# Kernel optimization log

Hardware: AMD Instinct MI355X
Metric: run time of the kernel (lower is better)

Reference implementation:

```python
import jax, jax.numpy as jnp
import numpy as np

NHEAD = 16
NEG = -1e9


def sinusoidal_pe(L, D):
    pos = jnp.arange(L, dtype=jnp.float32)[:, None]
    i = jnp.arange(0, D, 2, dtype=jnp.float32)[None, :]
    angle = pos / jnp.power(10000.0, i / D)
    pe = jnp.zeros((L, D), dtype=jnp.float32)
    pe = pe.at[:, 0::2].set(jnp.sin(angle))
    pe = pe.at[:, 1::2].set(jnp.cos(angle))
    return pe


def layer_norm(x, g, b, eps=1e-5):
    m = jnp.mean(x, axis=-1, keepdims=True)
    v = jnp.var(x, axis=-1, keepdims=True)
    return (x - m) * jax.lax.rsqrt(v + eps) * g + b


def build_mixed_mask_local(utt_mask, spk_mask, window, bidirectional=True):
    # utt_mask, spk_mask: [L] ints. Returns three [L, L] bool masks (True = attend).
    L = utt_mask.shape[0]
    idx = jnp.arange(L)
    d = idx[None, :] - idx[:, None]  # j - i
    if bidirectional:
        win = jnp.abs(d) <= window
    else:
        win = (d <= 0) & (d >= -window)
    valid = (utt_mask[None, :] > 0) & (utt_mask[:, None] > 0)
    base = win & valid
    same = spk_mask[None, :] == spk_mask[:, None]
    eye = jnp.eye(L, dtype=bool)
    uttm = base
    samm = base & same
    othm = base & (~same | eye)  # keep self so no query row is fully masked
    return uttm, samm, othm


def encoder_branch(x, bias, Wqkv, bqkv, Wo, bo, g1, b1, Wf1, bf1, Wf2, bf2, g2, b2):
    # x: [L, D]; bias: [L, L] additive mask; stacked per-layer params (leading dim = num_layer)
    num_layer = Wqkv.shape[0]
    L, D = x.shape
    dh = D // NHEAD
    scale = 1.0 / np.sqrt(dh).astype(np.float32)
    for l in range(num_layer):
        qkv = x @ Wqkv[l] + bqkv[l]                       # [L, 3D]
        q, k, v = jnp.split(qkv, 3, axis=-1)
        q = q.reshape(L, NHEAD, dh).transpose(1, 0, 2)    # [H, L, dh]
        k = k.reshape(L, NHEAD, dh).transpose(1, 0, 2)
        v = v.reshape(L, NHEAD, dh).transpose(1, 0, 2)
        s = jnp.einsum('hqd,hkd->hqk', q, k) * scale + bias[None]  # [H, L, L]
        a = jax.nn.softmax(s, axis=-1)
        o = jnp.einsum('hqk,hkd->hqd', a, v).transpose(1, 0, 2).reshape(L, D)
        x = layer_norm(x + o @ Wo[l] + bo[l], g1[l], b1[l])
        f = jax.nn.relu(x @ Wf1[l] + bf1[l]) @ Wf2[l] + bf2[l]
        x = layer_norm(x + f, g2[l], b2[l])
    return x


def fusion_attention(h, W, b, v):
    # h: [K, L, D] -> attention weights over K branch dim
    s = jnp.tanh(h @ W + b) @ v          # [K, L]
    w = jax.nn.softmax(s, axis=0)
    return jnp.einsum('kl,kld->ld', w, h)


def _xavier(key, shape):
    s = np.sqrt(2.0 / (shape[-2] + shape[-1])).astype(np.float32)
    return jax.random.normal(key, shape, dtype=jnp.float32) * s


def setup_inputs() -> dict:
    L, D, DF, NL, C = 1024, 1024, 4096, 3, 7
    key = jax.random.key(0)
    ks = jax.random.split(key, 12)
    return {
        'src': jax.random.normal(ks[0], (L, D), dtype=jnp.float32),
        'utt_mask': jnp.ones((L,), dtype=jnp.int32),
        'spk_mask': jax.random.randint(ks[1], (L,), 0, 2),
        'window': 100,
        'Wqkv': _xavier(ks[2], (3, NL, D, 3 * D)),
        'bqkv': jnp.zeros((3, NL, 3 * D), jnp.float32),
        'Wo': _xavier(ks[3], (3, NL, D, D)),
        'bo': jnp.zeros((3, NL, D), jnp.float32),
        'ln1_g': jnp.ones((3, NL, D), jnp.float32),
        'ln1_b': jnp.zeros((3, NL, D), jnp.float32),
        'Wf1': _xavier(ks[4], (3, NL, D, DF)),
        'bf1': jnp.zeros((3, NL, DF), jnp.float32),
        'Wf2': _xavier(ks[5], (3, NL, DF, D)),
        'bf2': jnp.zeros((3, NL, D), jnp.float32),
        'ln2_g': jnp.ones((3, NL, D), jnp.float32),
        'ln2_b': jnp.zeros((3, NL, D), jnp.float32),
        'f1_W': _xavier(ks[6], (D, D)),
        'f1_b': jnp.zeros((D,), jnp.float32),
        'f1_v': jax.random.normal(ks[7], (D,), dtype=jnp.float32) * 0.02,
        'f2_W': _xavier(ks[8], (D, D)),
        'f2_b': jnp.zeros((D,), jnp.float32),
        'f2_v': jax.random.normal(ks[9], (D,), dtype=jnp.float32) * 0.02,
        'cls_W': _xavier(ks[10], (D, C)),
        'cls_b': jnp.zeros((C,), jnp.float32),
    }


def reference(src, utt_mask, spk_mask, window, Wqkv, bqkv, Wo, bo, ln1_g, ln1_b,
              Wf1, bf1, Wf2, bf2, ln2_g, ln2_b, f1_W, f1_b, f1_v,
              f2_W, f2_b, f2_v, cls_W, cls_b):
    L, D = src.shape
    uttm, samm, othm = build_mixed_mask_local(utt_mask, spk_mask, window, bidirectional=True)
    bias = jnp.where(jnp.stack([uttm, samm, othm]), 0.0, NEG)  # [3, L, L]
    x = src + sinusoidal_pe(L, D)
    outs = jax.vmap(encoder_branch, in_axes=(None, 0, 0, 0, 0, 0, 0, 0, 0, 0, 0, 0, 0, 0))(
        x, bias, Wqkv, bqkv, Wo, bo, ln1_g, ln1_b, Wf1, bf1, Wf2, bf2, ln2_g, ln2_b)
    ct, sm, om = outs[0], outs[1], outs[2]
    sp = fusion_attention(jnp.stack([sm, om]), f1_W, f1_b, f1_v)
    out = fusion_attention(jnp.stack([ct, sp]), f2_W, f2_b, f2_v)
    return jax.nn.log_softmax(out @ cls_W + cls_b, axis=-1)
```

## Files before the change

### kernel.cpp

```cpp
#include <hip/hip_runtime.h>
#include <cmath>

namespace {

constexpr int L   = 1024;
constexpr int D   = 1024;
constexpr int DFF = 4096;
constexpr int NL  = 3;
constexpr int NH  = 16;
constexpr int DH  = 64;
constexpr long LD = (long)L * D;

typedef __attribute__((ext_vector_type(8))) short bf16x8;
typedef __attribute__((ext_vector_type(4))) float f32x4;

__device__ inline void split1(float f, unsigned short& h, unsigned short& l)
{
    unsigned u = __float_as_uint(f);
    h = (unsigned short)(u >> 16);
    float hf = __uint_as_float(u & 0xffff0000u);
    l = (unsigned short)(__float_as_uint(f - hf) >> 16);
}

__device__ inline void xcd_decode(int& bx, int& by, int& bz)
{
    const int gx = gridDim.x, gy = gridDim.y;
    const int nwg = gx * gy * gridDim.z;
    int flat = blockIdx.x + gx * (blockIdx.y + gy * blockIdx.z);
    int w = (flat & 7) * (nwg >> 3) + (flat >> 3);
    bz = w / (gx * gy);
    int rem = w - bz * gx * gy;
    by = rem / gx;
    bx = rem - by * gx;
}

__global__ __launch_bounds__(256)
void repack_w(const float* __restrict__ W, int ldw, long sW,
              unsigned short* __restrict__ out, long sOut, int Np)
{
    const int t    = threadIdx.x;
    const int lane = t & 63;
    const int c    = blockIdx.x * 4 + (t >> 6);
    const int z    = blockIdx.y;
    const int nch  = Np >> 4;
    const int k0   = (c / nch) * 32 + ((lane >> 4) << 3);
    const int n    = (c % nch) * 16 + (lane & 15);
    const float* Wz = W + (long)z * sW + n;
    unsigned short* oz = out + (long)z * sOut + (long)c * 1024 + (lane << 3);
    unsigned short h[8], l[8];
#pragma unroll
    for (int e = 0; e < 8; ++e)
        split1(Wz[(long)(k0 + e) * ldw], h[e], l[e]);
    *(ushort4*)(oz)       = *(ushort4*)&h[0];
    *(ushort4*)(oz + 4)   = *(ushort4*)&h[4];
    *(ushort4*)(oz + 512) = *(ushort4*)&l[0];
    *(ushort4*)(oz + 516) = *(ushort4*)&l[4];
}

template<int BM, int BN, int ACT>
__global__ __launch_bounds__(256)
void gemm_mfma_pb(const float* __restrict__ A, int lda, long sA,
                  const unsigned short* __restrict__ Bp, int Np, long sBp,
                  float* __restrict__ C, int ldc, long sC,
                  const float* __restrict__ bias, long sBias,
                  int K, float alpha, int ksl, long sSlice)
{
    constexpr int BK = 32;
    constexpr int PK = 40;
    constexpr int FM = BM / 32;
    constexpr int FN = BN / 32;
    constexpr int NA = BM / 32;

    __shared__ __align__(16) unsigned short Ah0[BM][PK], Al0[BM][PK];
    __shared__ __align__(16) unsigned short Ah1[BM][PK], Al1[BM][PK];

    int bx, by, bz;
    xcd_decode(bx, by, bz);
    const int zb = bz / ksl, ks = bz - zb * ksl;
    const int kLen = K / ksl, k0 = ks * kLen;
    const int nit = kLen / BK;

    const int tid  = threadIdx.x;
    const int lane = tid & 63;
    const int wave = tid >> 6;
    const int wm   = (wave >> 1) * (BM / 2);
    const int wn   = (wave & 1)  * (BN / 2);
    const int lr   = lane & 15;
    const int ko   = (lane >> 4) * 8;

    const float* Abase = A + (long)zb * sA;
    const unsigned short* Bb = Bp + (long)zb * sBp;
    float* Cbase = C + (long)zb * sC + (long)ks * sSlice;
    const int n0  = bx * BN;
    const int m0  = by * BM;
    const int nch = Np >> 4;
    const int cb  = (n0 + wn) >> 4;

    f32x4 acc[FM][FN];
#pragma unroll
    for (int i = 0; i < FM; ++i)
#pragma unroll
        for (int j = 0; j < FN; ++j) acc[i][j] = f32x4{0.f, 0.f, 0.f, 0.f};

    const int akq = tid & 7;
    const int amr = tid >> 3;

    auto loadA = [&](int kt, float4* pa) {
#pragma unroll
        for (int r = 0; r < NA; ++r)
            pa[r] = *(const float4*)(Abase + (long)(m0 + r * 32 + amr) * lda + kt + akq * 4);
    };
    auto storeA = [&](unsigned short (*AhD)[PK], unsigned short (*AlD)[PK],
                      const float4* pa) {
#pragma unroll
        for (int r = 0; r < NA; ++r) {
            ushort4 h, l;
            split1(pa[r].x, h.x, l.x); split1(pa[r].y, h.y, l.y);
            split1(pa[r].z, h.z, l.z); split1(pa[r].w, h.w, l.w);
            *(ushort4*)&AhD[r * 32 + amr][akq * 4] = h;
            *(ushort4*)&AlD[r * 32 + amr][akq * 4] = l;
        }
    };
    auto loadB = [&](int kt, bf16x8* h, bf16x8* l) {
        const unsigned short* p = Bb + ((long)(kt >> 5) * nch + cb) * 1024 + (lane << 3);
#pragma unroll
        for (int ni = 0; ni < FN; ++ni) {
            h[ni] = *(const bf16x8*)(p + ni * 1024);
            l[ni] = *(const bf16x8*)(p + ni * 1024 + 512);
        }
    };
    auto mmaStep = [&](unsigned short (*AhS)[PK], unsigned short (*AlS)[PK],
                       const bf16x8* bh, const bf16x8* bl) {
        bf16x8 ah[FM], al[FM];
#pragma unroll
        for (int mi = 0; mi < FM; ++mi) {
            ah[mi] = *(const bf16x8*)&AhS[wm + mi * 16 + lr][ko];
            al[mi] = *(const bf16x8*)&AlS[wm + mi * 16 + lr][ko];
        }
#pragma unroll
        for (int mi = 0; mi < FM; ++mi)
#pragma unroll
            for (int ni = 0; ni < FN; ++ni) {
                acc[mi][ni] = __builtin_amdgcn_mfma_f32_16x16x32_bf16(
                    ah[mi], bh[ni], acc[mi][ni], 0, 0, 0);
                acc[mi][ni] = __builtin_amdgcn_mfma_f32_16x16x32_bf16(
                    ah[mi], bl[ni], acc[mi][ni], 0, 0, 0);
                acc[mi][ni] = __builtin_amdgcn_mfma_f32_16x16x32_bf16(
                    al[mi], bh[ni], acc[mi][ni], 0, 0, 0);
            }
    };
    auto bar = [&]() {
        asm volatile("s_waitcnt lgkmcnt(0)" ::: "memory");
        __builtin_amdgcn_s_barrier();
    };

    float4 paA[NA], paB[NA];
    bf16x8 bhE[FN], blE[FN], bhO[FN], blO[FN];

    loadA(k0, paA);
    loadB(k0, bhE, blE);
    loadA(k0 + BK, paB);
    storeA(Ah0, Al0, paA);
    loadB(k0 + BK, bhO, blO);
    bar();

    for (int t = 0; t < nit; t += 2) {
        if (t + 2 < nit) loadA(k0 + (t + 2) * BK, paA);
        mmaStep(Ah0, Al0, bhE, blE);
        if (t + 2 < nit) loadB(k0 + (t + 2) * BK, bhE, blE);
        storeA(Ah1, Al1, paB);
        bar();
        if (t + 3 < nit) loadA(k0 + (t + 3) * BK, paB);
        mmaStep(Ah1, Al1, bhO, blO);
        if (t + 3 < nit) loadB(k0 + (t + 3) * BK, bhO, blO);
        if (t + 2 < nit) {
            storeA(Ah0, Al0, paA);
            bar();
        }
    }

    float bv[FN];
#pragma unroll
    for (int ni = 0; ni < FN; ++ni)
        bv[ni] = (bias && ks == 0)
               ? bias[(long)zb * sBias + n0 + wn + ni * 16 + lr] : 0.f;
    const int cr = (lane >> 4) * 4;
#pragma unroll
    for (int mi = 0; mi < FM; ++mi)
#pragma unroll
        for (int ni = 0; ni < FN; ++ni) {
#pragma unroll
            for (int r = 0; r < 4; ++r) {
                float t = acc[mi][ni][r] * alpha + bv[ni];
                if (ACT == 1) t = fmaxf(t, 0.f);
                else if (ACT == 2) t = tanhf(t);
                Cbase[(long)(m0 + wm + mi * 16 + cr + r) * ldc
                      + n0 + wn + ni * 16 + lr] = t;
            }
        }
}

template<int BM, int BN, int ACT, bool BT, int MODE>
__global__ __launch_bounds__(256)
void gemm_mfma(const float* __restrict__ A, int lda, long sA,
               const float* __restrict__ B, int ldb, long sB,
               float* __restrict__ C, int ldc, long sC,
               const float* __restrict__ bias, long sBias,
               int K, float alpha, const int* __restrict__ winp)
{
    constexpr int BK = 32;
    constexpr int PK = 40;
    constexpr int FM = BM / 32;
    constexpr int FN = BN / 32;
    constexpr int NA = BM / 32;
    constexpr int NB = BN / 32;

    __shared__ __align__(16) unsigned short Ah[BM][PK], Al[BM][PK];
    __shared__ __align__(16) unsigned short Bh[BN][PK], Bl[BN][PK];

    int bx, by, bz;
    xcd_decode(bx, by, bz);

    const int n0 = bx * BN;
    const int m0 = by * BM;

    int klo = 0, khi = K;
    if constexpr (MODE == 1) {
        const int w = winp[0];
        if (n0 > m0 + (BM - 1) + w || m0 > n0 + (BN - 1) + w) return;
    } else if constexpr (MODE == 2) {
        const int w = winp[0];
        klo = (m0 > w) ? ((m0 - w) & ~31) : 0;
        khi = (m0 + BM + w + 31) & ~31;
        if (khi > K) khi = K;
    }

    const int tid  = threadIdx.x;
    const int lane = tid & 63;
    const int wave = tid >> 6;
    const int wm   = (wave >> 1) * (BM / 2);
    const int wn   = (wave & 1)  * (BN / 2);
    const int lr   = lane & 15;
    const int ko   = (lane >> 4) * 8;

    const float* Abase = A + (long)bz * sA;
    const float* Bbase = B + (long)bz * sB;
    float*       Cbase = C + (long)bz * sC;

    f32x4 acc[FM][FN];
#pragma unroll
    for (int i = 0; i < FM; ++i)
#pragma unroll
        for (int j = 0; j < FN; ++j) acc[i][j] = f32x4{0.f, 0.f, 0.f, 0.f};

    const int akq = tid & 7;
    const int amr = tid >> 3;

    auto loadA = [&](int kt, float4* pa) {
#pragma unroll
        for (int r = 0; r < NA; ++r)
            pa[r] = *(const float4*)(Abase + (long)(m0 + r * 32 + amr) * lda + kt + akq * 4);
    };
    auto loadB = [&](int kt, float4* pb) {
#pragma unroll
        for (int r = 0; r < NB; ++r)
            pb[r] = *(const float4*)(Bbase + (long)(n0 + r * 32 + amr) * ldb + kt + akq * 4);
    };
    auto storeA = [&](const float4* pa) {
#pragma unroll
        for (int r = 0; r < NA; ++r) {
            ushort4 h, l;
            split1(pa[r].x, h.x, l.x); split1(pa[r].y, h.y, l.y);
            split1(pa[r].z, h.z, l.z); split1(pa[r].w, h.w, l.w);
            *(ushort4*)&Ah[r * 32 + amr][akq * 4] = h;
            *(ushort4*)&Al[r * 32 + amr][akq * 4] = l;
        }
    };
    auto storeB = [&](const float4* pb) {
#pragma unroll
        for (int r = 0; r < NB; ++r) {
            ushort4 h, l;
            split1(pb[r].x, h.x, l.x); split1(pb[r].y, h.y, l.y);
            split1(pb[r].z, h.z, l.z); split1(pb[r].w, h.w, l.w);
            *(ushort4*)&Bh[r * 32 + amr][akq * 4] = h;
            *(ushort4*)&Bl[r * 32 + amr][akq * 4] = l;
        }
    };

    float4 pa[NA], pb[NB];
    loadA(klo, pa); loadB(klo, pb);

    for (int kt = klo; kt < khi; kt += BK) {
        storeA(pa);
        storeB(pb);
        __syncthreads();

        const bool more = kt + BK < khi;
        float4 na[NA], nb[NB];
        if (more) { loadA(kt + BK, na); loadB(kt + BK, nb); }

        bf16x8 ah[FM], al[FM], bh[FN], bl[FN];
#pragma unroll
        for (int mi = 0; mi < FM; ++mi) {
            ah[mi] = *(const bf16x8*)&Ah[wm + mi * 16 + lr][ko];
            al[mi] = *(const bf16x8*)&Al[wm + mi * 16 + lr][ko];
        }
#pragma unroll
        for (int ni = 0; ni < FN; ++ni) {
            bh[ni] = *(const bf16x8*)&Bh[wn + ni * 16 + lr][ko];
            bl[ni] = *(const bf16x8*)&Bl[wn + ni * 16 + lr][ko];
        }
#pragma unroll
        for (int mi = 0; mi < FM; ++mi)
#pragma unroll
            for (int ni = 0; ni < FN; ++ni) {
                acc[mi][ni] = __builtin_amdgcn_mfma_f32_16x16x32_bf16(
                    ah[mi], bh[ni], acc[mi][ni], 0, 0, 0);
                acc[mi][ni] = __builtin_amdgcn_mfma_f32_16x16x32_bf16(
                    ah[mi], bl[ni], acc[mi][ni], 0, 0, 0);
                acc[mi][ni] = __builtin_amdgcn_mfma_f32_16x16x32_bf16(
                    al[mi], bh[ni], acc[mi][ni], 0, 0, 0);
            }
        __syncthreads();

        if (more) {
#pragma unroll
            for (int r = 0; r < NA; ++r) pa[r] = na[r];
#pragma unroll
            for (int r = 0; r < NB; ++r) pb[r] = nb[r];
        }
    }

    float bv[FN];
#pragma unroll
    for (int ni = 0; ni < FN; ++ni)
        bv[ni] = bias ? bias[(long)bz * sBias + n0 + wn + ni * 16 + lr] : 0.f;
    const int cr = (lane >> 4) * 4;
#pragma unroll
    for (int mi = 0; mi < FM; ++mi)
#pragma unroll
        for (int ni = 0; ni < FN; ++ni) {
#pragma unroll
            for (int r = 0; r < 4; ++r) {
                float t = acc[mi][ni][r] * alpha + bv[ni];
                if (ACT == 1) t = fmaxf(t, 0.f);
                else if (ACT == 2) t = tanhf(t);
                Cbase[(long)(m0 + wm + mi * 16 + cr + r) * ldc
                      + n0 + wn + ni * 16 + lr] = t;
            }
        }
}

__global__ __launch_bounds__(256)
void vtrans_kernel(const float* __restrict__ qkv, float* __restrict__ vt)
{
    __shared__ float t[32][33];
    const int b  = blockIdx.z;
    const int l0 = blockIdx.x * 32, c0 = blockIdx.y * 32;
    const int tx = threadIdx.x & 31, ty = threadIdx.x >> 5;
    const float* src = qkv + (long)b * 3 * LD + 2048;
#pragma unroll
    for (int r = ty; r < 32; r += 8)
        t[r][tx] = src[(long)(l0 + r) * 3072 + c0 + tx];
    __syncthreads();
    float* dst = vt + (long)b * LD;
#pragma unroll
    for (int r = ty; r < 32; r += 8)
        dst[(long)(c0 + r) * L + l0 + tx] = t[tx][r];
}

__global__ void add_pe_kernel(const float* __restrict__ src, float* __restrict__ x)
{
    long idx = (long)blockIdx.x * 256 + threadIdx.x;
    int pos = (int)(idx >> 10);
    int d   = (int)(idx & 1023);
    float expnt = (float)(d & ~1) * (1.0f / (float)D);
    float denom = powf(10000.0f, expnt);
    float ang   = (float)pos / denom;
    float pe    = (d & 1) ? cosf(ang) : sinf(ang);
    float v = src[idx] + pe;
    x[idx]          = v;
    x[LD + idx]     = v;
    x[2 * LD + idx] = v;
}

__global__ __launch_bounds__(256)
void softmax_mask_kernel(float* __restrict__ S, const int* __restrict__ utt,
                         const int* __restrict__ spk, const int* __restrict__ winp,
                         int branch)
{
    __shared__ float red[8];
    const int i   = blockIdx.x;
    const int h   = blockIdx.y;
    const int tid = threadIdx.x;
    float* row = S + ((long)h * L + i) * L;
    const int w    = winp[0];
    const int ti   = i >> 6;
    const int kmin = (ti * 64 > w) ? (((ti * 64 - w) >> 5) << 5) : 0;
    int khi = (ti * 64 + 64 + w + 31) & ~31;
    if (khi > L) khi = L;
    const int utti = utt[i];
    const int spki = spk[i];
    const int j0 = kmin + tid * 4;
    const bool act = j0 < khi;

    float s[4] = {-1e9f, -1e9f, -1e9f, -1e9f};
    if (act) {
        float4 sv = *(float4*)(row + j0);
        float svv[4] = {sv.x, sv.y, sv.z, sv.w};
#pragma unroll
        for (int c = 0; c < 4; ++c) {
            int j = j0 + c;
            int dd = j - i;
            bool win  = (dd <= w) && (-dd <= w);
            bool base = win && (utti > 0) && (utt[j] > 0);
            bool same = (spk[j] == spki);
            bool keep = (branch == 0) ? base
                      : (branch == 1) ? (base && same)
                      : (base && (!same || (j == i)));
            s[c] = keep ? svv[c] : -1e9f;
        }
    }
    float mx = fmaxf(fmaxf(s[0], s[1]), fmaxf(s[2], s[3]));
    for (int off = 32; off; off >>= 1) mx = fmaxf(mx, __shfl_xor(mx, off));
    if ((tid & 63) == 0) red[tid >> 6] = mx;
    __syncthreads();
    mx = fmaxf(fmaxf(red[0], red[1]), fmaxf(red[2], red[3]));
    __syncthreads();

    float e[4]; float sum = 0.f;
#pragma unroll
    for (int c = 0; c < 4; ++c) { e[c] = expf(s[c] - mx); sum += e[c]; }
    for (int off = 32; off; off >>= 1) sum += __shfl_xor(sum, off);
    if ((tid & 63) == 0) red[tid >> 6] = sum;
    __syncthreads();
    float inv = 1.f / (red[0] + red[1] + red[2] + red[3]);

    if (act) {
        float4 o = {e[0] * inv, e[1] * inv, e[2] * inv, e[3] * inv};
        *(float4*)(row + j0) = o;
    }
}

__global__ __launch_bounds__(256)
void ln_kernel(const float* __restrict__ x, const float* __restrict__ r,
               int nslc, long sSlice,
               const float* __restrict__ g, const float* __restrict__ b,
               float* __restrict__ out, long paramStride)
{
    __shared__ float red[8];
    const int row = blockIdx.x;
    const int grp = row >> 10;
    const int tid = threadIdx.x;
    const long base = (long)row * D + tid * 4;

    float4 t = *(const float4*)(x + base);
    for (int s = 0; s < nslc; ++s) {
        float4 rv = *(const float4*)(r + (long)s * sSlice + base);
        t.x += rv.x; t.y += rv.y; t.z += rv.z; t.w += rv.w;
    }

    float sm = t.x + t.y + t.z + t.w;
    for (int off = 32; off; off >>= 1) sm += __shfl_xor(sm, off);
    if ((tid & 63) == 0) red[tid >> 6] = sm;
    __syncthreads();
    float mean = (red[0] + red[1] + red[2] + red[3]) * (1.f / (float)D);
    __syncthreads();

    float4 dv = {t.x - mean, t.y - mean, t.z - mean, t.w - mean};
    float sq = dv.x * dv.x + dv.y * dv.y + dv.z * dv.z + dv.w * dv.w;
    for (int off = 32; off; off >>= 1) sq += __shfl_xor(sq, off);
    if ((tid & 63) == 0) red[tid >> 6] = sq;
    __syncthreads();
    float var  = (red[0] + red[1] + red[2] + red[3]) * (1.f / (float)D);
    float rstd = rsqrtf(var + 1e-5f);

    const float* gp = g + (long)grp * paramStride + tid * 4;
    const float* bp = b + (long)grp * paramStride + tid * 4;
    float4 gv = *(const float4*)gp;
    float4 bv = *(const float4*)bp;
    float4 o = {dv.x * rstd * gv.x + bv.x, dv.y * rstd * gv.y + bv.y,
                dv.z * rstd * gv.z + bv.z, dv.w * rstd * gv.w + bv.w};
    *(float4*)(out + base) = o;
}

__global__ __launch_bounds__(256)
void rowdot_kernel(const float* __restrict__ t, long sSlice, int nslc,
                   const float* __restrict__ v, float* __restrict__ s)
{
    __shared__ float red[8];
    const int row = blockIdx.x;
    const int tid = threadIdx.x;
    const long base = (long)row * D + tid * 4;
    float4 a = *(const float4*)(t + base);
    for (int sl = 1; sl < nslc; ++sl) {
        float4 a2 = *(const float4*)(t + (long)sl * sSlice + base);
        a.x += a2.x; a.y += a2.y; a.z += a2.z; a.w += a2.w;
    }
    a.x = tanhf(a.x); a.y = tanhf(a.y); a.z = tanhf(a.z); a.w = tanhf(a.w);
    float4 vv = *(const float4*)(v + tid * 4);
    float p = a.x * vv.x + a.y * vv.y + a.z * vv.z + a.w * vv.w;
    for (int off = 32; off; off >>= 1) p += __shfl_xor(p, off);
    if ((tid & 63) == 0) red[tid >> 6] = p;
    __syncthreads();
    if (tid == 0) s[row] = red[0] + red[1] + red[2] + red[3];
}

__global__ void combine_kernel(const float* __restrict__ sb, const float* __restrict__ h,
                               float* __restrict__ out)
{
    long idx = (long)blockIdx.x * 256 + threadIdx.x;
    int l = (int)(idx >> 10);
    float s0 = sb[l], s1 = sb[L + l];
    float m  = fmaxf(s0, s1);
    float e0 = expf(s0 - m), e1 = expf(s1 - m);
    float inv = 1.f / (e0 + e1);
    out[idx] = (e0 * h[idx] + e1 * h[LD + idx]) * inv;
}

__global__ __launch_bounds__(256)
void cls_kernel(const float* __restrict__ x, const float* __restrict__ W,
                const float* __restrict__ b, float* __restrict__ out)
{
    __shared__ float red[4][7];
    __shared__ float logit[7];
    const int row = blockIdx.x;
    const int tid = threadIdx.x;
    float p[7] = {0, 0, 0, 0, 0, 0, 0};
    for (int d = tid; d < D; d += 256) {
        float xv = x[(long)row * D + d];
#pragma unroll
        for (int c = 0; c < 7; ++c) p[c] = fmaf(xv, W[d * 7 + c], p[c]);
    }
#pragma unroll
    for (int c = 0; c < 7; ++c) {
        float v = p[c];
        for (int off = 32; off; off >>= 1) v += __shfl_xor(v, off);
        if ((tid & 63) == 0) red[tid >> 6][c] = v;
    }
    __syncthreads();
    if (tid < 7)
        logit[tid] = red[0][tid] + red[1][tid] + red[2][tid] + red[3][tid] + b[tid];
    __syncthreads();
    if (tid == 0) {
        float mx = logit[0];
        for (int c = 1; c < 7; ++c) mx = fmaxf(mx, logit[c]);
        float sum = 0.f;
        for (int c = 0; c < 7; ++c) sum += expf(logit[c] - mx);
        float lse = logf(sum) + mx;
        for (int c = 0; c < 7; ++c) out[(long)row * 7 + c] = logit[c] - lse;
    }
}

}

extern "C" void kernel_launch(void* const* d_in, const int* in_sizes, int n_in,
                              void* d_out, int out_size, void* d_ws, size_t ws_size,
                              hipStream_t stream)
{
    (void)in_sizes; (void)n_in; (void)out_size; (void)ws_size;

    const float* src  = (const float*)d_in[0];
    const int*   utt  = (const int*)d_in[1];
    const int*   spk  = (const int*)d_in[2];
    const int*   winp = (const int*)d_in[3];
    const float* Wqkv = (const float*)d_in[4];
    const float* bqkv = (const float*)d_in[5];
    const float* Wo   = (const float*)d_in[6];
    const float* bo   = (const float*)d_in[7];
    const float* g1   = (const float*)d_in[8];
    const float* b1   = (const float*)d_in[9];
    const float* Wf1  = (const float*)d_in[10];
    const float* bf1  = (const float*)d_in[11];
    const float* Wf2  = (const float*)d_in[12];
    const float* bf2  = (const float*)d_in[13];
    const float* g2   = (const float*)d_in[14];
    const float* b2   = (const float*)d_in[15];
    const float* f1W  = (const float*)d_in[16];
    const float* f1b  = (const float*)d_in[17];
    const float* f1v  = (const float*)d_in[18];
    const float* f2W  = (const float*)d_in[19];
    const float* f2b  = (const float*)d_in[20];
    const float* f2v  = (const float*)d_in[21];
    const float* clsW = (const float*)d_in[22];
    const float* clsb = (const float*)d_in[23];
    float* out = (float*)d_out;

    float* ws    = (float*)d_ws;
    float* x     = ws;
    float* qkv   = x + 3 * LD;
    float* attno = qkv + 9 * LD;
    float* tmp   = attno + 3 * LD;
    float* R1    = tmp + 3 * LD;
    float* sbuf  = R1 + 16 * LD;
    float* S    = R1;
    float* ffn  = R1;
    float* vt   = tmp;
    float* f2s  = qkv;
    float* h2   = R1 + 4 * LD;
    unsigned short* wpack = (unsigned short*)(sbuf + 2 * L);

    add_pe_kernel<<<LD / 256, 256, 0, stream>>>(src, x);

    for (int l = 0; l < NL; ++l) {
        repack_w<<<dim3(6144 / 4, 3), 256, 0, stream>>>(
            Wqkv + (long)l * D * 3 * D, 3 * D, (long)NL * D * 3 * D,
            wpack, (long)2 * D * 3 * D, 3 * D);
        gemm_mfma_pb<128, 128, 0>
            <<<dim3(3 * D / 128, L / 128, 3), 256, 0, stream>>>(
            x, D, LD, wpack, 3 * D, (long)2 * D * 3 * D,
            qkv, 3 * D, 3 * LD, bqkv + (long)l * 3 * D, (long)NL * 3 * D,
            D, 1.f, 1, 0);

        vtrans_kernel<<<dim3(L / 32, D / 32, 3), 256, 0, stream>>>(qkv, vt);

        for (int b = 0; b < 3; ++b) {
            const float* qkvb = qkv + (long)b * 3 * LD;
            gemm_mfma<128, 128, 0, true, 1>
                <<<dim3(L / 128, L / 128, NH), 256, 0, stream>>>(
                qkvb, 3 * D, 64, qkvb + D, 3 * D, 64,
                S, L, (long)L * L, nullptr, 0, DH, 0.125f, winp);
            softmax_mask_kernel<<<dim3(L, NH), 256, 0, stream>>>(S, utt, spk, winp, b);
            gemm_mfma<64, 64, 0, true, 2>
                <<<dim3(1, L / 64, NH), 256, 0, stream>>>(
                S, L, (long)L * L, vt + (long)b * LD, L, (long)64 * L,
                attno + (long)b * LD, D, 64, nullptr, 0, L, 1.f, winp);
        }

        repack_w<<<dim3(2048 / 4, 3), 256, 0, stream>>>(
            Wo + (long)l * D * D, D, (long)NL * D * D,
            wpack, (long)2 * D * D, D);
        gemm_mfma_pb<128, 128, 0>
            <<<dim3(D / 128, L / 128, 12), 256, 0, stream>>>(
            attno, D, LD, wpack, D, (long)2 * D * D,
            R1, D, LD, bo + (long)l * D, (long)NL * D,
            D, 1.f, 4, (long)3 * LD);
        ln_kernel<<<3 * L, 256, 0, stream>>>(x, R1, 4, (long)3 * LD,
                                             g1 + (long)l * D, b1 + (long)l * D,
                                             x, (long)NL * D);
        repack_w<<<dim3(8192 / 4, 3), 256, 0, stream>>>(
            Wf1 + (long)l * D * DFF, DFF, (long)NL * D * DFF,
            wpack, (long)2 * D * DFF, DFF);
        gemm_mfma_pb<128, 128, 1>
            <<<dim3(DFF / 128, L / 128, 3), 256, 0, stream>>>(
            x, D, LD, wpack, DFF, (long)2 * D * DFF,
            ffn, DFF, (long)L * DFF, bf1 + (long)l * DFF, (long)NL * DFF,
            D, 1.f, 1, 0);
        repack_w<<<dim3(8192 / 4, 3), 256, 0, stream>>>(
            Wf2 + (long)l * DFF * D, D, (long)NL * DFF * D,
            wpack, (long)2 * DFF * D, D);
        gemm_mfma_pb<128, 128, 0>
            <<<dim3(D / 128, L / 128, 12), 256, 0, stream>>>(
            ffn, DFF, (long)L * DFF, wpack, D, (long)2 * DFF * D,
            f2s, D, LD, bf2 + (long)l * D, (long)NL * D,
            DFF, 1.f, 4, (long)3 * LD);
        ln_kernel<<<3 * L, 256, 0, stream>>>(x, f2s, 4, (long)3 * LD,
                                             g2 + (long)l * D, b2 + (long)l * D,
                                             x, (long)NL * D);
    }

    repack_w<<<dim3(2048 / 4, 1), 256, 0, stream>>>(f1W, D, 0, wpack, 0, D);
    gemm_mfma_pb<128, 128, 0>
        <<<dim3(D / 128, L / 128, 4), 256, 0, stream>>>(
        x + LD, D, LD, wpack, D, 0, R1, D, LD, f1b, 0, D, 1.f, 2, (long)2 * LD);
    rowdot_kernel<<<2 * L, 256, 0, stream>>>(R1, (long)2 * LD, 2, f1v, sbuf);
    combine_kernel<<<LD / 256, 256, 0, stream>>>(sbuf, x + LD, h2 + LD);
    hipMemcpyAsync(h2, x, LD * sizeof(float), hipMemcpyDeviceToDevice, stream);

    repack_w<<<dim3(2048 / 4, 1), 256, 0, stream>>>(f2W, D, 0, wpack, 0, D);
    gemm_mfma_pb<128, 128, 0>
        <<<dim3(D / 128, L / 128, 4), 256, 0, stream>>>(
        h2, D, LD, wpack, D, 0, R1, D, LD, f2b, 0, D, 1.f, 2, (long)2 * LD);
    rowdot_kernel<<<2 * L, 256, 0, stream>>>(R1, (long)2 * LD, 2, f2v, sbuf);
    combine_kernel<<<LD / 256, 256, 0, stream>>>(sbuf, h2, tmp);

    cls_kernel<<<L, 256, 0, stream>>>(tmp, clsW, clsb, out);
}
```

Baseline: 2.270 ms.

## Widen packed GEMM tiles to 128x256, single-buffer B fragments, tile repack through LDS

The packed-weight GEMM now uses 128x256 tiles, doubling N-tile width so each A tile staged in LDS is reused across more columns. B fragments are single-buffered in registers, A fragments are loaded per row-block, and launch bounds request two blocks per CU, all to keep register pressure manageable with the wider tile. The weight repack kernel now reads a 32x128 tile with coalesced float4 loads into LDS before splitting into bf16 hi/lo, replacing strided column reads. The trade-off is less B prefetch overlap and fewer blocks per grid, which can hurt latency hiding and CU occupancy on the smaller GEMMs.

After: 1.903 ms. -16.2%, faster.

```diff
diff --git a/kernel.cpp b/kernel.cpp
--- a/kernel.cpp
+++ b/kernel.cpp
@@ -38,27 +38,41 @@
 void repack_w(const float* __restrict__ W, int ldw, long sW,
               unsigned short* __restrict__ out, long sOut, int Np)
 {
-    const int t    = threadIdx.x;
-    const int lane = t & 63;
-    const int c    = blockIdx.x * 4 + (t >> 6);
-    const int z    = blockIdx.y;
-    const int nch  = Np >> 4;
-    const int k0   = (c / nch) * 32 + ((lane >> 4) << 3);
-    const int n    = (c % nch) * 16 + (lane & 15);
-    const float* Wz = W + (long)z * sW + n;
-    unsigned short* oz = out + (long)z * sOut + (long)c * 1024 + (lane << 3);
-    unsigned short h[8], l[8];
-#pragma unroll
-    for (int e = 0; e < 8; ++e)
-        split1(Wz[(long)(k0 + e) * ldw], h[e], l[e]);
-    *(ushort4*)(oz)       = *(ushort4*)&h[0];
-    *(ushort4*)(oz + 4)   = *(ushort4*)&h[4];
-    *(ushort4*)(oz + 512) = *(ushort4*)&l[0];
-    *(ushort4*)(oz + 516) = *(ushort4*)&l[4];
+    __shared__ float lds[32][129];
+    const int t = threadIdx.x;
+    const int ntile = Np >> 7;
+    const int kt = blockIdx.x / ntile, nt = blockIdx.x % ntile;
+    const int z = blockIdx.y;
+    const float* Wz = W + (long)z * sW + (long)(kt * 32) * ldw + nt * 128;
+    const int q = t & 31, rg = t >> 5;
+#pragma unroll
+    for (int i = 0; i < 4; ++i) {
+        int r = rg * 4 + i;
+        *(float4*)&lds[r][q * 4] = *(const float4*)(Wz + (long)r * ldw + q * 4);
+    }
+    __syncthreads();
+    const int lane = t & 63, wave = t >> 6;
+    const int nch = Np >> 4;
+#pragma unroll
+    for (int j = 0; j < 2; ++j) {
+        int ci = wave * 2 + j;
+        int n  = ci * 16 + (lane & 15);
+        int oct = lane >> 4;
+        unsigned short h[8], l[8];
+#pragma unroll
+        for (int e = 0; e < 8; ++e)
+            split1(lds[oct * 8 + e][n], h[e], l[e]);
+        unsigned short* oz = out + (long)z * sOut
+            + ((long)kt * nch + nt * 8 + ci) * 1024 + (lane << 3);
+        *(ushort4*)(oz)       = *(ushort4*)&h[0];
+        *(ushort4*)(oz + 4)   = *(ushort4*)&h[4];
+        *(ushort4*)(oz + 512) = *(ushort4*)&l[0];
+        *(ushort4*)(oz + 516) = *(ushort4*)&l[4];
+    }
 }
 
 template<int BM, int BN, int ACT>
-__global__ __launch_bounds__(256)
+__global__ __launch_bounds__(256, 2)
 void gemm_mfma_pb(const float* __restrict__ A, int lda, long sA,
                   const unsigned short* __restrict__ Bp, int Np, long sBp,
                   float* __restrict__ C, int ldc, long sC,
@@ -131,23 +145,20 @@
     };
     auto mmaStep = [&](unsigned short (*AhS)[PK], unsigned short (*AlS)[PK],
                        const bf16x8* bh, const bf16x8* bl) {
-        bf16x8 ah[FM], al[FM];
 #pragma unroll
         for (int mi = 0; mi < FM; ++mi) {
-            ah[mi] = *(const bf16x8*)&AhS[wm + mi * 16 + lr][ko];
-            al[mi] = *(const bf16x8*)&AlS[wm + mi * 16 + lr][ko];
-        }
-#pragma unroll
-        for (int mi = 0; mi < FM; ++mi)
+            bf16x8 ah = *(const bf16x8*)&AhS[wm + mi * 16 + lr][ko];
+            bf16x8 al = *(const bf16x8*)&AlS[wm + mi * 16 + lr][ko];
 #pragma unroll
             for (int ni = 0; ni < FN; ++ni) {
                 acc[mi][ni] = __builtin_amdgcn_mfma_f32_16x16x32_bf16(
-                    ah[mi], bh[ni], acc[mi][ni], 0, 0, 0);
+                    ah, bh[ni], acc[mi][ni], 0, 0, 0);
                 acc[mi][ni] = __builtin_amdgcn_mfma_f32_16x16x32_bf16(
-                    ah[mi], bl[ni], acc[mi][ni], 0, 0, 0);
+                    ah, bl[ni], acc[mi][ni], 0, 0, 0);
                 acc[mi][ni] = __builtin_amdgcn_mfma_f32_16x16x32_bf16(
-                    al[mi], bh[ni], acc[mi][ni], 0, 0, 0);
+                    al, bh[ni], acc[mi][ni], 0, 0, 0);
             }
+        }
     };
     auto bar = [&]() {
         asm volatile("s_waitcnt lgkmcnt(0)" ::: "memory");
@@ -155,25 +166,24 @@
     };
 
     float4 paA[NA], paB[NA];
-    bf16x8 bhE[FN], blE[FN], bhO[FN], blO[FN];
+    bf16x8 bh[FN], bl[FN];
 
     loadA(k0, paA);
-    loadB(k0, bhE, blE);
+    loadB(k0, bh, bl);
     loadA(k0 + BK, paB);
     storeA(Ah0, Al0, paA);
-    loadB(k0 + BK, bhO, blO);
     bar();
 
     for (int t = 0; t < nit; t += 2) {
         if (t + 2 < nit) loadA(k0 + (t + 2) * BK, paA);
-        mmaStep(Ah0, Al0, bhE, blE);
-        if (t + 2 < nit) loadB(k0 + (t + 2) * BK, bhE, blE);
+        mmaStep(Ah0, Al0, bh, bl);
+        if (t + 1 < nit) loadB(k0 + (t + 1) * BK, bh, bl);
         storeA(Ah1, Al1, paB);
         bar();
         if (t + 3 < nit) loadA(k0 + (t + 3) * BK, paB);
-        mmaStep(Ah1, Al1, bhO, blO);
-        if (t + 3 < nit) loadB(k0 + (t + 3) * BK, bhO, blO);
+        mmaStep(Ah1, Al1, bh, bl);
         if (t + 2 < nit) {
+            loadB(k0 + (t + 2) * BK, bh, bl);
             storeA(Ah0, Al0, paA);
             bar();
         }
@@ -603,11 +613,11 @@
     add_pe_kernel<<<LD / 256, 256, 0, stream>>>(src, x);
 
     for (int l = 0; l < NL; ++l) {
-        repack_w<<<dim3(6144 / 4, 3), 256, 0, stream>>>(
+        repack_w<<<dim3(32 * 24, 3), 256, 0, stream>>>(
             Wqkv + (long)l * D * 3 * D, 3 * D, (long)NL * D * 3 * D,
             wpack, (long)2 * D * 3 * D, 3 * D);
-        gemm_mfma_pb<128, 128, 0>
-            <<<dim3(3 * D / 128, L / 128, 3), 256, 0, stream>>>(
+        gemm_mfma_pb<128, 256, 0>
+            <<<dim3(3 * D / 256, L / 128, 3), 256, 0, stream>>>(
             x, D, LD, wpack, 3 * D, (long)2 * D * 3 * D,
             qkv, 3 * D, 3 * LD, bqkv + (long)l * 3 * D, (long)NL * 3 * D,
             D, 1.f, 1, 0);
@@ -627,30 +637,30 @@
                 attno + (long)b * LD, D, 64, nullptr, 0, L, 1.f, winp);
         }
 
-        repack_w<<<dim3(2048 / 4, 3), 256, 0, stream>>>(
+        repack_w<<<dim3(32 * 8, 3), 256, 0, stream>>>(
             Wo + (long)l * D * D, D, (long)NL * D * D,
             wpack, (long)2 * D * D, D);
-        gemm_mfma_pb<128, 128, 0>
-            <<<dim3(D / 128, L / 128, 12), 256, 0, stream>>>(
+        gemm_mfma_pb<128, 256, 0>
+            <<<dim3(D / 256, L / 128, 12), 256, 0, stream>>>(
             attno, D, LD, wpack, D, (long)2 * D * D,
             R1, D, LD, bo + (long)l * D, (long)NL * D,
             D, 1.f, 4, (long)3 * LD);
         ln_kernel<<<3 * L, 256, 0, stream>>>(x, R1, 4, (long)3 * LD,
                                              g1 + (long)l * D, b1 + (long)l * D,
                                              x, (long)NL * D);
-        repack_w<<<dim3(8192 / 4, 3), 256, 0, stream>>>(
+        repack_w<<<dim3(32 * 32, 3), 256, 0, stream>>>(
             Wf1 + (long)l * D * DFF, DFF, (long)NL * D * DFF,
             wpack, (long)2 * D * DFF, DFF);
-        gemm_mfma_pb<128, 128, 1>
-            <<<dim3(DFF / 128, L / 128, 3), 256, 0, stream>>>(
+        gemm_mfma_pb<128, 256, 1>
+            <<<dim3(DFF / 256, L / 128, 3), 256, 0, stream>>>(
             x, D, LD, wpack, DFF, (long)2 * D * DFF,
             ffn, DFF, (long)L * DFF, bf1 + (long)l * DFF, (long)NL * DFF,
             D, 1.f, 1, 0);
-        repack_w<<<dim3(8192 / 4, 3), 256, 0, stream>>>(
+        repack_w<<<dim3(128 * 8, 3), 256, 0, stream>>>(
             Wf2 + (long)l * DFF * D, D, (long)NL * DFF * D,
             wpack, (long)2 * DFF * D, D);
-        gemm_mfma_pb<128, 128, 0>
-            <<<dim3(D / 128, L / 128, 12), 256, 0, stream>>>(
+        gemm_mfma_pb<128, 256, 0>
+            <<<dim3(D / 256, L / 128, 12), 256, 0, stream>>>(
             ffn, DFF, (long)L * DFF, wpack, D, (long)2 * DFF * D,
             f2s, D, LD, bf2 + (long)l * D, (long)NL * D,
             DFF, 1.f, 4, (long)3 * LD);
@@ -659,17 +669,17 @@
                                              x, (long)NL * D);
     }
 
-    repack_w<<<dim3(2048 / 4, 1), 256, 0, stream>>>(f1W, D, 0, wpack, 0, D);
-    gemm_mfma_pb<128, 128, 0>
-        <<<dim3(D / 128, L / 128, 4), 256, 0, stream>>>(
+    repack_w<<<dim3(32 * 8, 1), 256, 0, stream>>>(f1W, D, 0, wpack, 0, D);
+    gemm_mfma_pb<128, 256, 0>
+        <<<dim3(D / 256, L / 128, 4), 256, 0, stream>>>(
         x + LD, D, LD, wpack, D, 0, R1, D, LD, f1b, 0, D, 1.f, 2, (long)2 * LD);
     rowdot_kernel<<<2 * L, 256, 0, stream>>>(R1, (long)2 * LD, 2, f1v, sbuf);
     combine_kernel<<<LD / 256, 256, 0, stream>>>(sbuf, x + LD, h2 + LD);
     hipMemcpyAsync(h2, x, LD * sizeof(float), hipMemcpyDeviceToDevice, stream);
 
-    repack_w<<<dim3(2048 / 4, 1), 256, 0, stream>>>(f2W, D, 0, wpack, 0, D);
-    gemm_mfma_pb<128, 128, 0>
-        <<<dim3(D / 128, L / 128, 4), 256, 0, stream>>>(
+    repack_w<<<dim3(32 * 8, 1), 256, 0, stream>>>(f2W, D, 0, wpack, 0, D);
+    gemm_mfma_pb<128, 256, 0>
+        <<<dim3(D / 256, L / 128, 4), 256, 0, stream>>>(
         h2, D, LD, wpack, D, 0, R1, D, LD, f2b, 0, D, 1.f, 2, (long)2 * LD);
     rowdot_kernel<<<2 * L, 256, 0, stream>>>(R1, (long)2 * LD, 2, f2v, sbuf);
     combine_kernel<<<LD / 256, 256, 0, stream>>>(sbuf, h2, tmp);
```
